# Optimization experiments

Hardware: AMD Instinct MI355X
Metric: run time of the kernel (lower is better)

Reference implementation:

```python
import jax, jax.numpy as jnp
import numpy as np

CH = 256
RED = 4
CQK = CH // RED

def _conv(x, w, b):
    # x: [B,C,H,W], w: [O,I,3,3], b: [O]; SAME padding (pad=1)
    y = jax.lax.conv_general_dilated(
        x, w, window_strides=(1, 1), padding=((1, 1), (1, 1)),
        dimension_numbers=('NCHW', 'OIHW', 'NCHW'))
    return y + b[None, :, None, None]

def setup_inputs() -> dict:
    key = jax.random.key(0)
    ks = jax.random.split(key, 7)
    x = jax.random.normal(ks[0], (4, CH, 64, 64), dtype=jnp.float32)
    fan_in = CH * 9
    s = 1.0 / np.sqrt(fan_in)
    q_w = jax.random.uniform(ks[1], (CQK, CH, 3, 3), jnp.float32, -s, s)
    q_b = jax.random.uniform(ks[2], (CQK,), jnp.float32, -s, s)
    k_w = jax.random.uniform(ks[3], (CQK, CH, 3, 3), jnp.float32, -s, s)
    k_b = jax.random.uniform(ks[4], (CQK,), jnp.float32, -s, s)
    v_w = jax.random.uniform(ks[5], (CH, CH, 3, 3), jnp.float32, -s, s)
    v_b = jax.random.uniform(ks[6], (CH,), jnp.float32, -s, s)
    return {"x": x, "q_w": q_w, "q_b": q_b, "k_w": k_w, "k_b": k_b,
            "v_w": v_w, "v_b": v_b}

def reference(x, q_w, q_b, k_w, k_b, v_w, v_b):
    b, c, h, w = x.shape
    hw = h * w
    scale = CQK ** (-0.5)
    q = _conv(x, q_w, q_b).reshape(b, CQK, hw)   # [B, Cqk, HW]
    k = _conv(x, k_w, k_b).reshape(b, CQK, hw)   # [B, Cqk, HW]
    v = _conv(x, v_w, v_b).reshape(b, c, hw)     # [B, C,   HW]
    # attn[b,i,j] = sum_d q[b,d,i] * k[b,d,j]
    attn = jnp.einsum('bdi,bdj->bij', q, k) * scale
    attn = jax.nn.softmax(attn, axis=-1)         # [B, HW, HW]
    # out[b,c,i] = sum_j v[b,c,j] * attn[b,i,j]  (torch: bmm(v, attn^T))
    out = jnp.einsum('bcj,bij->bci', v, attn).reshape(b, c, h, w)
    return out
```

## Files before the change

### kernel.cpp

```cpp
#include <hip/hip_runtime.h>
#include <stdint.h>

typedef unsigned short u16;
typedef short short8 __attribute__((ext_vector_type(8)));
typedef short short4v __attribute__((ext_vector_type(4)));
typedef float float4v __attribute__((ext_vector_type(4)));
typedef float float16v __attribute__((ext_vector_type(16)));
typedef uint32_t uint2v __attribute__((ext_vector_type(2)));

#define HW 4096
#define QSCL 0.18033688011112042f

#define GLOAD_LDS(g, l) __builtin_amdgcn_global_load_lds( \
    (const __attribute__((address_space(1))) void*)(g),   \
    (__attribute__((address_space(3))) void*)(l), 16, 0, 0)

static __device__ __forceinline__ u16 f2bf(float f) {
  union { float f; uint32_t u; } v; v.f = f;
  uint32_t r = v.u + 0x7fffu + ((v.u >> 16) & 1u);
  return (u16)(r >> 16);
}

static __device__ __forceinline__ uint32_t pkbf(float a, float b) {
  uint32_t r;
  asm("v_cvt_pk_bf16_f32 %0, %1, %2" : "=v"(r) : "v"(a), "v"(b));
  return r;
}
static __device__ __forceinline__ void plswap(uint32_t &a, uint32_t &b) {
  asm("v_permlane32_swap_b32 %0, %1" : "+v"(a), "+v"(b));
}

union PU { uint32_t u[4]; short8 v; };

__global__ __launch_bounds__(256) void k_xt(const float* __restrict__ x, u16* __restrict__ Xtp) {
  __shared__ float t[32][33];
  const int b = blockIdx.z, c0 = blockIdx.y * 32, p0 = blockIdx.x * 32;
  const int tid = threadIdx.x;
  const int l8 = tid >> 5, lp = tid & 31;
#pragma unroll
  for (int i = 0; i < 4; i++) {
    int c = l8 + i * 8;
    t[c][lp] = x[(size_t)(b * 256 + c0 + c) * HW + p0 + lp];
  }
  __syncthreads();
#pragma unroll
  for (int i = 0; i < 4; i++) {
    int p = l8 + i * 8;
    int pp = p0 + p;
    int y = pp >> 6, xx = pp & 63;
    Xtp[((size_t)(b * 66 + y + 1) * 66 + (xx + 1)) * 256 + c0 + lp] = f2bf(t[lp][p]);
  }
}

__global__ __launch_bounds__(256) void k_wprep(const float* __restrict__ qw, const float* __restrict__ qb,
    const float* __restrict__ kw, const float* __restrict__ kb,
    const float* __restrict__ vw, const float* __restrict__ vb,
    u16* __restrict__ Wt, float* __restrict__ bcat) {
  int tid = blockIdx.x * 256 + threadIdx.x;
  if (tid < 9 * 384 * 256) {
    int ci = tid & 255;
    int n = (tid >> 8) % 384;
    int off = tid / (384 * 256);
    float val;
    if (n < 64)       val = qw[(size_t)n * 2304 + ci * 9 + off];
    else if (n < 128) val = kw[(size_t)(n - 64) * 2304 + ci * 9 + off];
    else              val = vw[(size_t)(n - 128) * 2304 + ci * 9 + off];
    Wt[tid] = f2bf(val);
  }
  if (tid < 384) bcat[tid] = (tid < 64) ? qb[tid] : (tid < 128) ? kb[tid - 64] : vb[tid - 128];
}

__global__ __launch_bounds__(256) void k_conv(const u16* __restrict__ Xtp,
    const u16* __restrict__ Wt, const float* __restrict__ bcat,
    u16* __restrict__ Qt, u16* __restrict__ Kt, u16* __restrict__ Vcf) {
  __shared__ __align__(16) u16 Als[2][128 * 64];
  __shared__ __align__(16) u16 Bls[2][64 * 64];
  const int tid = threadIdx.x;
  const int b = blockIdx.z, ct = blockIdx.y;
  const int p0 = blockIdx.x * 128, n0 = ct * 64;
  const int w = tid >> 6, lane = tid & 63, l16 = lane & 15, quad = lane >> 4;

  const int lr = lane >> 3, lcx = (lane & 7) ^ lr;
  const u16* ag[4];
#pragma unroll
  for (int g = 0; g < 4; g++) {
    const int pos = p0 + w * 32 + g * 8 + lr;
    const int py = pos >> 6, px = pos & 63;
    ag[g] = Xtp + ((size_t)(b * 66 + py) * 66 + px) * 256 + lcx * 8;
  }
  const u16* bg[2];
#pragma unroll
  for (int g = 0; g < 2; g++)
    bg[g] = Wt + (size_t)(n0 + w * 16 + g * 8 + lr) * 256 + lcx * 8;

  const int rx = l16 & 7;

  float4v acc[2][4];
  const float4v zz = {0.f, 0.f, 0.f, 0.f};
#pragma unroll
  for (int i = 0; i < 2; i++)
#pragma unroll
    for (int j = 0; j < 4; j++) acc[i][j] = zz;

#pragma unroll
  for (int g = 0; g < 4; g++) GLOAD_LDS(ag[g], &Als[0][(w * 32 + g * 8) * 64]);
#pragma unroll
  for (int g = 0; g < 2; g++) GLOAD_LDS(bg[g], &Bls[0][(w * 16 + g * 8) * 64]);
  __syncthreads();

  for (int ks = 0; ks < 36; ks++) {
    const int buf = ks & 1;
    if (ks + 1 < 36) {
      const int ksn = ks + 1, tap = ksn >> 2, cg = (ksn & 3) * 64;
      const int dy = (tap * 11) >> 5, dx = tap - dy * 3;
      const int aoff = (dy * 66 + dx) * 256 + cg;
      const size_t boff = (size_t)tap * 98304 + cg;
#pragma unroll
      for (int g = 0; g < 4; g++) GLOAD_LDS(ag[g] + aoff, &Als[buf ^ 1][(w * 32 + g * 8) * 64]);
#pragma unroll
      for (int g = 0; g < 2; g++) GLOAD_LDS(bg[g] + boff, &Bls[buf ^ 1][(w * 16 + g * 8) * 64]);
    }

    short8 af[2][2], bfv[4][2];
#pragma unroll
    for (int mt = 0; mt < 2; mt++)
#pragma unroll
      for (int kk = 0; kk < 2; kk++)
        af[mt][kk] = *(const short8*)&Als[buf][(w * 32 + mt * 16 + l16) * 64 + (((kk * 4 + quad) ^ rx) * 8)];
#pragma unroll
    for (int nt = 0; nt < 4; nt++)
#pragma unroll
      for (int kk = 0; kk < 2; kk++)
        bfv[nt][kk] = *(const short8*)&Bls[buf][(nt * 16 + l16) * 64 + (((kk * 4 + quad) ^ rx) * 8)];

    if (ct < 2) {
#pragma unroll
      for (int mt = 0; mt < 2; mt++)
#pragma unroll
        for (int nt = 0; nt < 4; nt++)
#pragma unroll
          for (int kk = 0; kk < 2; kk++)
            acc[mt][nt] = __builtin_amdgcn_mfma_f32_16x16x32_bf16(bfv[nt][kk], af[mt][kk], acc[mt][nt], 0, 0, 0);
    } else {
#pragma unroll
      for (int mt = 0; mt < 2; mt++)
#pragma unroll
        for (int nt = 0; nt < 4; nt++)
#pragma unroll
          for (int kk = 0; kk < 2; kk++)
            acc[mt][nt] = __builtin_amdgcn_mfma_f32_16x16x32_bf16(af[mt][kk], bfv[nt][kk], acc[mt][nt], 0, 0, 0);
    }
    __syncthreads();
  }

  if (ct < 2) {
    u16* base = (ct == 0) ? Qt : Kt;
    const float qs = (ct == 0) ? QSCL : 1.0f;
#pragma unroll
    for (int mt = 0; mt < 2; mt++) {
      const int p = p0 + w * 32 + mt * 16 + l16;
#pragma unroll
      for (int nt = 0; nt < 4; nt++) {
        const int nb = nt * 16 + quad * 4;
        short4v o;
#pragma unroll
        for (int r = 0; r < 4; r++) o[r] = (short)f2bf((acc[mt][nt][r] + bcat[ct * 64 + nb + r]) * qs);
        *(short4v*)(base + (size_t)(b * HW + p) * 64 + nb) = o;
      }
    }
  } else {
#pragma unroll
    for (int mt = 0; mt < 2; mt++) {
      const int pb = p0 + w * 32 + mt * 16 + quad * 4;
#pragma unroll
      for (int nt = 0; nt < 4; nt++) {
        const int cl = nt * 16 + l16;
        const int gc = (ct - 2) * 64 + cl;
        const float bias = bcat[ct * 64 + cl];
        short4v o;
#pragma unroll
        for (int r = 0; r < 4; r++) o[r] = (short)f2bf(acc[mt][nt][r] + bias);
        *(short4v*)(Vcf + (size_t)(b * 256 + gc) * HW + pb) = o;
      }
    }
  }
}

__global__ __launch_bounds__(256, 1) void k_attn(const u16* __restrict__ Qt,
    const u16* __restrict__ Kt, const u16* __restrict__ Vcf, float* __restrict__ out) {
  __shared__ __align__(16) u16 lds[61440];

  const int tid = threadIdx.x;
  const int bid = blockIdx.x;
  const int b = bid & 3;
  const int w = tid >> 6, lane = tid & 63;
  const int l32 = lane & 31, half = lane >> 5;
  const int qa = w & 1, jh = w >> 1;
  const int q0 = (bid >> 2) * 64 + qa * 32;

  u16* Sb = lds + jh * 30720;

  const char* Kgb = (const char*)(Kt + (size_t)b * HW * 64);
  const char* Vgb = (const char*)(Vcf + (size_t)b * 256 * HW);

  const int lr = lane >> 3, lcx = (lane & 7) ^ lr;
  const int vr = lane >> 2, vcx = (lane & 3) ^ ((lane >> 3) & 3);
  const char* ksrc = Kgb + ((size_t)(jh * 2048 + qa * 16 + lr)) * 128 + lcx * 16;
  const char* vsrc = Vgb + ((size_t)(qa * 128 + vr)) * 8192 + (size_t)(jh * 2048) * 2 + vcx * 16;

  short8 qf[4];
  {
    const u16* qp = Qt + ((size_t)(b * HW + q0 + l32)) * 64 + half * 8;
#pragma unroll
    for (int ks = 0; ks < 4; ks++) qf[ks] = *(const short8*)(qp + ks * 16);
  }

  const int sw2 = (l32 >> 1) & 3;
  const int kswz = l32 & 7;

  float16v of[8];
#pragma unroll
  for (int ct = 0; ct < 8; ct++)
#pragma unroll
    for (int r = 0; r < 16; r++) of[ct][r] = 0.f;
  float lp = 0.f;

#define STAGE(T, KS, VS) {                                                        \
    const size_t kb_ = (size_t)(T) * 4096;                                        \
    const size_t vb_ = (size_t)(T) * 64;                                          \
    _Pragma("unroll") for (int g = 0; g < 2; g++)                                 \
      GLOAD_LDS(ksrc + kb_ + g * 1024, &Sb[(KS) + qa * 1024 + g * 512]);          \
    _Pragma("unroll") for (int g = 0; g < 8; g++)                                 \
      GLOAD_LDS(vsrc + vb_ + (size_t)g * 131072, &Sb[(VS) + qa * 4096 + g * 512]);\
  }

#define COMPUTE() {                                                               \
    float16v s;                                                                   \
    _Pragma("unroll") for (int r = 0; r < 16; r++) s[r] = 0.f;                    \
    _Pragma("unroll") for (int ks = 0; ks < 4; ks++) {                            \
      short8 kf = *(const short8*)&Sb[kc + l32 * 64 + (((ks * 2 + half) ^ kswz) * 8)]; \
      s = __builtin_amdgcn_mfma_f32_32x32x16_bf16(kf, qf[ks], s, 0, 0, 0);        \
    }                                                                             \
    float p[16];                                                                  \
    _Pragma("unroll") for (int r = 0; r < 16; r++) p[r] = exp2f(s[r]);            \
    _Pragma("unroll") for (int r = 0; r < 16; r++) lp += p[r];                    \
    uint32_t c0 = pkbf(p[0], p[1]),  c1 = pkbf(p[2], p[3]);                       \
    uint32_t c2 = pkbf(p[4], p[5]),  c3 = pkbf(p[6], p[7]);                       \
    plswap(c0, c2); plswap(c1, c3);                                               \
    uint32_t d0 = pkbf(p[8], p[9]),  d1 = pkbf(p[10], p[11]);                     \
    uint32_t d2 = pkbf(p[12], p[13]), d3 = pkbf(p[14], p[15]);                    \
    plswap(d0, d2); plswap(d1, d3);                                               \
    PU pb0, pb1;                                                                  \
    pb0.u[0] = c0; pb0.u[1] = c1; pb0.u[2] = c2; pb0.u[3] = c3;                   \
    pb1.u[0] = d0; pb1.u[1] = d1; pb1.u[2] = d2; pb1.u[3] = d3;                   \
    _Pragma("unroll") for (int ct = 0; ct < 8; ct++) {                            \
      short8 vf0 = *(const short8*)&Sb[vc + ct * 1024 + l32 * 32 + ((half ^ sw2) * 8)]; \
      of[ct] = __builtin_amdgcn_mfma_f32_32x32x16_bf16(vf0, pb0.v, of[ct], 0, 0, 0);   \
      short8 vf1 = *(const short8*)&Sb[vc + ct * 1024 + l32 * 32 + (((2 + half) ^ sw2) * 8)]; \
      of[ct] = __builtin_amdgcn_mfma_f32_32x32x16_bf16(vf1, pb1.v, of[ct], 0, 0, 0);   \
    }                                                                             \
  }

  int kc = 0, kn = 2048, kt2 = 4096;
  int vc = 6144, vn = 6144 + 8192, vt2 = 6144 + 16384;

  STAGE(0, kc, vc);
  STAGE(1, kn, vn);

  for (int t = 0; t < 63; t++) {
    asm volatile("s_waitcnt vmcnt(10)" ::: "memory");
    __builtin_amdgcn_s_barrier();
    if (t < 62) STAGE(t + 2, kt2, vt2);
    COMPUTE();
    int tk = kc; kc = kn; kn = kt2; kt2 = tk;
    int tv = vc; vc = vn; vn = vt2; vt2 = tv;
  }
  asm volatile("s_waitcnt vmcnt(0)" ::: "memory");
  __builtin_amdgcn_s_barrier();
  COMPUTE();

#undef STAGE
#undef COMPUTE

  lp += __shfl_xor(lp, 32);
  __syncthreads();
  float* Lf = (float*)(lds + 30720);
  if (lane < 32) Lf[w * 32 + l32] = lp;
  float* Osh = (float*)(lds + qa * 30720 + 6144);
  if (jh) {
#pragma unroll
    for (int ct = 0; ct < 8; ct++)
#pragma unroll
      for (int r = 0; r < 16; r++)
        Osh[(ct * 32 + (r & 3) + 8 * (r >> 2) + 4 * half) * 32 + l32] = of[ct][r];
  }
  __syncthreads();
  if (!jh) {
    const float inv = 1.0f / (Lf[qa * 32 + l32] + Lf[(2 + qa) * 32 + l32]);
    float* ob = out + (size_t)b * 256 * HW + q0 + l32;
#pragma unroll
    for (int ct = 0; ct < 8; ct++)
#pragma unroll
      for (int r = 0; r < 16; r++) {
        const int c = ct * 32 + (r & 3) + 8 * (r >> 2) + 4 * half;
        ob[(size_t)c * HW] = (of[ct][r] + Osh[c * 32 + l32]) * inv;
      }
  }
}

extern "C" void kernel_launch(void* const* d_in, const int* in_sizes, int n_in,
                              void* d_out, int out_size, void* d_ws, size_t ws_size,
                              hipStream_t stream) {
  const float* x  = (const float*)d_in[0];
  const float* qw = (const float*)d_in[1];
  const float* qb = (const float*)d_in[2];
  const float* kw = (const float*)d_in[3];
  const float* kb = (const float*)d_in[4];
  const float* vw = (const float*)d_in[5];
  const float* vb = (const float*)d_in[6];
  float* out = (float*)d_out;
  char* ws = (char*)d_ws;
  u16*   Xtp = (u16*)(ws);
  u16*   Wt  = (u16*)(ws + 8921088);
  float* bc  = (float*)(ws + 10690560);
  u16*   Qt  = (u16*)(ws + 10692096);
  u16*   Kt  = (u16*)(ws + 12789248);
  u16*   Vcf = (u16*)(ws + 14886400);

  hipMemsetAsync(Xtp, 0, 8921088, stream);
  k_xt  <<<dim3(128, 8, 4), 256, 0, stream>>>(x, Xtp);
  k_wprep<<<3456, 256, 0, stream>>>(qw, qb, kw, kb, vw, vb, Wt, bc);
  k_conv<<<dim3(32, 6, 4), 256, 0, stream>>>(Xtp, Wt, bc, Qt, Kt, Vcf);
  k_attn<<<256, 256, 0, stream>>>(Qt, Kt, Vcf, out);
}
```

Measured before the change: 194.5 us.

## Load K fragments directly to registers and double-buffer larger V tiles

Restructures the attention main loop. K fragments are now loaded straight from global memory into registers two tiles ahead, instead of being staged through LDS. Each iteration handles 64 keys, computing two score tiles, and only V goes through double-buffered LDS with an XOR swizzle. This halves the number of barriers per key range and removes K LDS traffic, at the cost of more registers for the K fragments and bigger V staging per step.

```diff
diff --git a/kernel.cpp b/kernel.cpp
--- a/kernel.cpp
+++ b/kernel.cpp
@@ -188,35 +188,33 @@
 
 __global__ __launch_bounds__(256, 1) void k_attn(const u16* __restrict__ Qt,
     const u16* __restrict__ Kt, const u16* __restrict__ Vcf, float* __restrict__ out) {
-  __shared__ __align__(16) u16 lds[61440];
+  __shared__ __align__(16) u16 lds[65536];
 
   const int tid = threadIdx.x;
   const int bid = blockIdx.x;
   const int b = bid & 3;
+  const int q0 = (bid >> 2) * 64;
   const int w = tid >> 6, lane = tid & 63;
   const int l32 = lane & 31, half = lane >> 5;
   const int qa = w & 1, jh = w >> 1;
-  const int q0 = (bid >> 2) * 64 + qa * 32;
-
-  u16* Sb = lds + jh * 30720;
-
-  const char* Kgb = (const char*)(Kt + (size_t)b * HW * 64);
-  const char* Vgb = (const char*)(Vcf + (size_t)b * 256 * HW);
+
+  u16* Sv = lds + jh * 32768;
 
   const int lr = lane >> 3, lcx = (lane & 7) ^ lr;
-  const int vr = lane >> 2, vcx = (lane & 3) ^ ((lane >> 3) & 3);
-  const char* ksrc = Kgb + ((size_t)(jh * 2048 + qa * 16 + lr)) * 128 + lcx * 16;
-  const char* vsrc = Vgb + ((size_t)(qa * 128 + vr)) * 8192 + (size_t)(jh * 2048) * 2 + vcx * 16;
+  const char* vs0 = (const char*)Vcf + ((size_t)(b * 256 + qa * 128 + lr)) * 8192
+                    + jh * 4096 + (size_t)lcx * 16;
+
+  const u16* kq = Kt + ((size_t)(b * HW + jh * 2048 + l32)) * 64 + half * 8;
 
   short8 qf[4];
   {
-    const u16* qp = Qt + ((size_t)(b * HW + q0 + l32)) * 64 + half * 8;
+    const u16* qp = Qt + ((size_t)(b * HW + q0 + qa * 32 + l32)) * 64 + half * 8;
 #pragma unroll
     for (int ks = 0; ks < 4; ks++) qf[ks] = *(const short8*)(qp + ks * 16);
   }
 
-  const int sw2 = (l32 >> 1) & 3;
-  const int kswz = l32 & 7;
+  const int rx = l32 & 7;
+  const int vrow = l32 * 64;
 
   float16v of[8];
 #pragma unroll
@@ -225,68 +223,83 @@
     for (int r = 0; r < 16; r++) of[ct][r] = 0.f;
   float lp = 0.f;
 
-#define STAGE(T, KS, VS) {                                                        \
-    const size_t kb_ = (size_t)(T) * 4096;                                        \
-    const size_t vb_ = (size_t)(T) * 64;                                          \
-    _Pragma("unroll") for (int g = 0; g < 2; g++)                                 \
-      GLOAD_LDS(ksrc + kb_ + g * 1024, &Sb[(KS) + qa * 1024 + g * 512]);          \
-    _Pragma("unroll") for (int g = 0; g < 8; g++)                                 \
-      GLOAD_LDS(vsrc + vb_ + (size_t)g * 131072, &Sb[(VS) + qa * 4096 + g * 512]);\
-  }
-
-#define COMPUTE() {                                                               \
-    float16v s;                                                                   \
-    _Pragma("unroll") for (int r = 0; r < 16; r++) s[r] = 0.f;                    \
+  short8 kfA[2][4], kfB[2][4];
+
+#define STAGEV(T, BUF) {                                                          \
+    const char* vt = vs0 + (size_t)(T) * 128;                                     \
+    u16* db = Sv + (BUF) * 16384 + qa * 8192;                                     \
+    _Pragma("unroll") for (int g = 0; g < 16; g++)                                \
+      GLOAD_LDS(vt + (size_t)g * 65536, db + g * 512);                            \
+  }
+
+#define LOADK(T, KF) {                                                            \
+    const u16* kp = kq + (size_t)((T) & 31) * 4096;                               \
+    _Pragma("unroll") for (int js = 0; js < 2; js++)                              \
+      _Pragma("unroll") for (int ks = 0; ks < 4; ks++)                            \
+        KF[js][ks] = *(const short8*)(kp + js * 2048 + ks * 16);                  \
+  }
+
+#define SOFTPV(SS, VB, C0, C1) {                                                  \
+    float p0 = exp2f(SS[0]),  p1 = exp2f(SS[1]),  p2 = exp2f(SS[2]),  p3 = exp2f(SS[3]);   \
+    float p4 = exp2f(SS[4]),  p5 = exp2f(SS[5]),  p6 = exp2f(SS[6]),  p7 = exp2f(SS[7]);   \
+    float p8 = exp2f(SS[8]),  p9 = exp2f(SS[9]),  pa = exp2f(SS[10]), pb_ = exp2f(SS[11]); \
+    float pc = exp2f(SS[12]), pd = exp2f(SS[13]), pe = exp2f(SS[14]), pf = exp2f(SS[15]);  \
+    lp += ((p0 + p1) + (p2 + p3)) + ((p4 + p5) + (p6 + p7))                       \
+        + ((p8 + p9) + (pa + pb_)) + ((pc + pd) + (pe + pf));                     \
+    uint32_t c0 = pkbf(p0, p1), c1 = pkbf(p2, p3), c2 = pkbf(p4, p5), c3 = pkbf(p6, p7);   \
+    plswap(c0, c2); plswap(c1, c3);                                               \
+    uint32_t d0 = pkbf(p8, p9), d1 = pkbf(pa, pb_), d2 = pkbf(pc, pd), d3 = pkbf(pe, pf);  \
+    plswap(d0, d2); plswap(d1, d3);                                               \
+    PU pA, pB;                                                                    \
+    pA.u[0] = c0; pA.u[1] = c1; pA.u[2] = c2; pA.u[3] = c3;                       \
+    pB.u[0] = d0; pB.u[1] = d1; pB.u[2] = d2; pB.u[3] = d3;                       \
+    const int ca = (((C0) + half) ^ rx) * 8, cb = (((C1) + half) ^ rx) * 8;       \
+    _Pragma("unroll") for (int ct = 0; ct < 8; ct++) {                            \
+      short8 vfa = *(const short8*)&VB[vrow + ct * 2048 + ca];                    \
+      of[ct] = __builtin_amdgcn_mfma_f32_32x32x16_bf16(vfa, pA.v, of[ct], 0, 0, 0); \
+      short8 vfb = *(const short8*)&VB[vrow + ct * 2048 + cb];                    \
+      of[ct] = __builtin_amdgcn_mfma_f32_32x32x16_bf16(vfb, pB.v, of[ct], 0, 0, 0); \
+    }                                                                             \
+  }
+
+#define HALF_ITER(T, PAR, KF) {                                                   \
+    asm volatile("s_waitcnt vmcnt(8)" ::: "memory");                              \
+    __builtin_amdgcn_s_barrier();                                                 \
+    __builtin_amdgcn_sched_barrier(0);                                            \
+    STAGEV(((T) + 1) & 31, (PAR) ^ 1);                                            \
+    __builtin_amdgcn_sched_barrier(0);                                            \
+    float16v s0, s1;                                                              \
+    _Pragma("unroll") for (int r = 0; r < 16; r++) { s0[r] = 0.f; s1[r] = 0.f; }  \
     _Pragma("unroll") for (int ks = 0; ks < 4; ks++) {                            \
-      short8 kf = *(const short8*)&Sb[kc + l32 * 64 + (((ks * 2 + half) ^ kswz) * 8)]; \
-      s = __builtin_amdgcn_mfma_f32_32x32x16_bf16(kf, qf[ks], s, 0, 0, 0);        \
+      s0 = __builtin_amdgcn_mfma_f32_32x32x16_bf16(KF[0][ks], qf[ks], s0, 0, 0, 0); \
+      s1 = __builtin_amdgcn_mfma_f32_32x32x16_bf16(KF[1][ks], qf[ks], s1, 0, 0, 0); \
     }                                                                             \
-    float p[16];                                                                  \
-    _Pragma("unroll") for (int r = 0; r < 16; r++) p[r] = exp2f(s[r]);            \
-    _Pragma("unroll") for (int r = 0; r < 16; r++) lp += p[r];                    \
-    uint32_t c0 = pkbf(p[0], p[1]),  c1 = pkbf(p[2], p[3]);                       \
-    uint32_t c2 = pkbf(p[4], p[5]),  c3 = pkbf(p[6], p[7]);                       \
-    plswap(c0, c2); plswap(c1, c3);                                               \
-    uint32_t d0 = pkbf(p[8], p[9]),  d1 = pkbf(p[10], p[11]);                     \
-    uint32_t d2 = pkbf(p[12], p[13]), d3 = pkbf(p[14], p[15]);                    \
-    plswap(d0, d2); plswap(d1, d3);                                               \
-    PU pb0, pb1;                                                                  \
-    pb0.u[0] = c0; pb0.u[1] = c1; pb0.u[2] = c2; pb0.u[3] = c3;                   \
-    pb1.u[0] = d0; pb1.u[1] = d1; pb1.u[2] = d2; pb1.u[3] = d3;                   \
-    _Pragma("unroll") for (int ct = 0; ct < 8; ct++) {                            \
-      short8 vf0 = *(const short8*)&Sb[vc + ct * 1024 + l32 * 32 + ((half ^ sw2) * 8)]; \
-      of[ct] = __builtin_amdgcn_mfma_f32_32x32x16_bf16(vf0, pb0.v, of[ct], 0, 0, 0);   \
-      short8 vf1 = *(const short8*)&Sb[vc + ct * 1024 + l32 * 32 + (((2 + half) ^ sw2) * 8)]; \
-      of[ct] = __builtin_amdgcn_mfma_f32_32x32x16_bf16(vf1, pb1.v, of[ct], 0, 0, 0);   \
-    }                                                                             \
-  }
-
-  int kc = 0, kn = 2048, kt2 = 4096;
-  int vc = 6144, vn = 6144 + 8192, vt2 = 6144 + 16384;
-
-  STAGE(0, kc, vc);
-  STAGE(1, kn, vn);
-
-  for (int t = 0; t < 63; t++) {
-    asm volatile("s_waitcnt vmcnt(10)" ::: "memory");
-    __builtin_amdgcn_s_barrier();
-    if (t < 62) STAGE(t + 2, kt2, vt2);
-    COMPUTE();
-    int tk = kc; kc = kn; kn = kt2; kt2 = tk;
-    int tv = vc; vc = vn; vn = vt2; vt2 = tv;
-  }
-  asm volatile("s_waitcnt vmcnt(0)" ::: "memory");
-  __builtin_amdgcn_s_barrier();
-  COMPUTE();
-
-#undef STAGE
-#undef COMPUTE
+    LOADK((T) + 2, KF);                                                           \
+    __builtin_amdgcn_sched_barrier(0);                                            \
+    const u16* VB = Sv + (PAR) * 16384;                                           \
+    SOFTPV(s0, VB, 0, 2);                                                         \
+    SOFTPV(s1, VB, 4, 6);                                                         \
+  }
+
+  STAGEV(0, 0);
+  __builtin_amdgcn_sched_barrier(0);
+  LOADK(0, kfA);
+  LOADK(1, kfB);
+
+  for (int t = 0; t < 32; t += 2) {
+    HALF_ITER(t, 0, kfA);
+    HALF_ITER(t + 1, 1, kfB);
+  }
+#undef HALF_ITER
+#undef SOFTPV
+#undef LOADK
+#undef STAGEV
 
   lp += __shfl_xor(lp, 32);
   __syncthreads();
-  float* Lf = (float*)(lds + 30720);
+  float* Lf = (float*)lds + 16384;
   if (lane < 32) Lf[w * 32 + l32] = lp;
-  float* Osh = (float*)(lds + qa * 30720 + 6144);
+  float* Osh = (float*)lds + qa * 8192;
   if (jh) {
 #pragma unroll
     for (int ct = 0; ct < 8; ct++)
@@ -297,7 +310,7 @@
   __syncthreads();
   if (!jh) {
     const float inv = 1.0f / (Lf[qa * 32 + l32] + Lf[(2 + qa) * 32 + l32]);
-    float* ob = out + (size_t)b * 256 * HW + q0 + l32;
+    float* ob = out + (size_t)(b * 256) * HW + q0 + qa * 32 + l32;
 #pragma unroll
     for (int ct = 0; ct < 8; ct++)
 #pragma unroll
```

New measurement: 225.2 us. +15.7%, slower.

## Split attention key range across blocks and reduce partial outputs in a separate kernel

Applied to the files above, without the earlier changes.

The attention kernel now launches 512 blocks of 512 threads. Each block handles one batch, one half of the key range and 64 queries, and each wave owns 64 output channels instead of all 256. The much smaller per-wave accumulator should allow higher occupancy with double-buffered LDS. Partial unnormalized outputs and row sums are written to workspace and combined in a new reduce kernel. The cost is extra global traffic (about 32 MB of fp32 partials written and read back), one more launch, and the QK^T scores being recomputed for each channel group of waves.

```diff
diff --git a/kernel.cpp b/kernel.cpp
--- a/kernel.cpp
+++ b/kernel.cpp
@@ -186,126 +186,120 @@
   }
 }
 
-__global__ __launch_bounds__(256, 1) void k_attn(const u16* __restrict__ Qt,
-    const u16* __restrict__ Kt, const u16* __restrict__ Vcf, float* __restrict__ out) {
-  __shared__ __align__(16) u16 lds[61440];
-
-  const int tid = threadIdx.x;
-  const int bid = blockIdx.x;
+__global__ __launch_bounds__(512, 4) void k_attn(const u16* __restrict__ Qt,
+    const u16* __restrict__ Kt, const u16* __restrict__ Vcf,
+    float* __restrict__ Opart, float* __restrict__ Lpart) {
+  __shared__ __align__(16) u16 Vls[2][8192];
+  __shared__ __align__(16) u16 Kls[2][2048];
+
+  const int tid = threadIdx.x, bid = blockIdx.x;
   const int b = bid & 3;
+  const int jh = (bid >> 2) & 1, it = bid >> 3;
   const int w = tid >> 6, lane = tid & 63;
   const int l32 = lane & 31, half = lane >> 5;
-  const int qa = w & 1, jh = w >> 1;
-  const int q0 = (bid >> 2) * 64 + qa * 32;
-
-  u16* Sb = lds + jh * 30720;
-
-  const char* Kgb = (const char*)(Kt + (size_t)b * HW * 64);
-  const char* Vgb = (const char*)(Vcf + (size_t)b * 256 * HW);
-
+  const int qa = w & 1, cs = w >> 1;
+
+  const int vr = lane >> 2, vcx = (lane & 3) ^ (vr & 3);
   const int lr = lane >> 3, lcx = (lane & 7) ^ lr;
-  const int vr = lane >> 2, vcx = (lane & 3) ^ ((lane >> 3) & 3);
-  const char* ksrc = Kgb + ((size_t)(jh * 2048 + qa * 16 + lr)) * 128 + lcx * 16;
-  const char* vsrc = Vgb + ((size_t)(qa * 128 + vr)) * 8192 + (size_t)(jh * 2048) * 2 + vcx * 16;
+  const char* vsrc = (const char*)Vcf + ((size_t)(b * 256 + w * 32 + vr)) * 8192
+                     + jh * 4096 + vcx * 16;
+  const char* ksrc = (const char*)Kt + ((size_t)(b * HW + jh * 2048 + (w & 3) * 8 + lr)) * 128
+                     + lcx * 16;
 
   short8 qf[4];
   {
-    const u16* qp = Qt + ((size_t)(b * HW + q0 + l32)) * 64 + half * 8;
+    const u16* qp = Qt + ((size_t)(b * HW + it * 64 + qa * 32 + l32)) * 64 + half * 8;
 #pragma unroll
     for (int ks = 0; ks < 4; ks++) qf[ks] = *(const short8*)(qp + ks * 16);
   }
 
-  const int sw2 = (l32 >> 1) & 3;
-  const int kswz = l32 & 7;
-
-  float16v of[8];
-#pragma unroll
-  for (int ct = 0; ct < 8; ct++)
-#pragma unroll
-    for (int r = 0; r < 16; r++) of[ct][r] = 0.f;
+  const int rxk = l32 & 7, rxv = l32 & 3;
+  const int krow = l32 * 64;
+  const int vrow0 = (cs * 64 + l32) * 32;
+
+  float16v of0, of1;
+#pragma unroll
+  for (int r = 0; r < 16; r++) { of0[r] = 0.f; of1[r] = 0.f; }
   float lp = 0.f;
 
-#define STAGE(T, KS, VS) {                                                        \
-    const size_t kb_ = (size_t)(T) * 4096;                                        \
-    const size_t vb_ = (size_t)(T) * 64;                                          \
-    _Pragma("unroll") for (int g = 0; g < 2; g++)                                 \
-      GLOAD_LDS(ksrc + kb_ + g * 1024, &Sb[(KS) + qa * 1024 + g * 512]);          \
-    _Pragma("unroll") for (int g = 0; g < 8; g++)                                 \
-      GLOAD_LDS(vsrc + vb_ + (size_t)g * 131072, &Sb[(VS) + qa * 4096 + g * 512]);\
-  }
-
-#define COMPUTE() {                                                               \
+#define STAGE(T, BUF) {                                                           \
+    GLOAD_LDS(vsrc + (size_t)(T) * 64, &Vls[BUF][(w * 32) * 32]);                 \
+    GLOAD_LDS(vsrc + (size_t)(T) * 64 + 16 * 8192, &Vls[BUF][(w * 32 + 16) * 32]);\
+    GLOAD_LDS(ksrc + (size_t)(T) * 4096, &Kls[BUF][(w & 3) * 512]);               \
+  }
+
+#define COMPUTE(BUF) {                                                            \
     float16v s;                                                                   \
     _Pragma("unroll") for (int r = 0; r < 16; r++) s[r] = 0.f;                    \
     _Pragma("unroll") for (int ks = 0; ks < 4; ks++) {                            \
-      short8 kf = *(const short8*)&Sb[kc + l32 * 64 + (((ks * 2 + half) ^ kswz) * 8)]; \
+      short8 kf = *(const short8*)&Kls[BUF][krow + (((ks * 2 + half) ^ rxk) * 8)];\
       s = __builtin_amdgcn_mfma_f32_32x32x16_bf16(kf, qf[ks], s, 0, 0, 0);        \
     }                                                                             \
-    float p[16];                                                                  \
-    _Pragma("unroll") for (int r = 0; r < 16; r++) p[r] = exp2f(s[r]);            \
-    _Pragma("unroll") for (int r = 0; r < 16; r++) lp += p[r];                    \
-    uint32_t c0 = pkbf(p[0], p[1]),  c1 = pkbf(p[2], p[3]);                       \
-    uint32_t c2 = pkbf(p[4], p[5]),  c3 = pkbf(p[6], p[7]);                       \
+    float p0 = exp2f(s[0]),  p1 = exp2f(s[1]),  p2 = exp2f(s[2]),  p3 = exp2f(s[3]);   \
+    float p4 = exp2f(s[4]),  p5 = exp2f(s[5]),  p6 = exp2f(s[6]),  p7 = exp2f(s[7]);   \
+    float p8 = exp2f(s[8]),  p9 = exp2f(s[9]),  pa = exp2f(s[10]), pb_ = exp2f(s[11]); \
+    float pc = exp2f(s[12]), pd = exp2f(s[13]), pe = exp2f(s[14]), pf = exp2f(s[15]);  \
+    lp += ((p0 + p1) + (p2 + p3)) + ((p4 + p5) + (p6 + p7))                       \
+        + ((p8 + p9) + (pa + pb_)) + ((pc + pd) + (pe + pf));                     \
+    uint32_t c0 = pkbf(p0, p1), c1 = pkbf(p2, p3), c2 = pkbf(p4, p5), c3 = pkbf(p6, p7);   \
     plswap(c0, c2); plswap(c1, c3);                                               \
-    uint32_t d0 = pkbf(p[8], p[9]),  d1 = pkbf(p[10], p[11]);                     \
-    uint32_t d2 = pkbf(p[12], p[13]), d3 = pkbf(p[14], p[15]);                    \
+    uint32_t d0 = pkbf(p8, p9), d1 = pkbf(pa, pb_), d2 = pkbf(pc, pd), d3 = pkbf(pe, pf);  \
     plswap(d0, d2); plswap(d1, d3);                                               \
-    PU pb0, pb1;                                                                  \
-    pb0.u[0] = c0; pb0.u[1] = c1; pb0.u[2] = c2; pb0.u[3] = c3;                   \
-    pb1.u[0] = d0; pb1.u[1] = d1; pb1.u[2] = d2; pb1.u[3] = d3;                   \
-    _Pragma("unroll") for (int ct = 0; ct < 8; ct++) {                            \
-      short8 vf0 = *(const short8*)&Sb[vc + ct * 1024 + l32 * 32 + ((half ^ sw2) * 8)]; \
-      of[ct] = __builtin_amdgcn_mfma_f32_32x32x16_bf16(vf0, pb0.v, of[ct], 0, 0, 0);   \
-      short8 vf1 = *(const short8*)&Sb[vc + ct * 1024 + l32 * 32 + (((2 + half) ^ sw2) * 8)]; \
-      of[ct] = __builtin_amdgcn_mfma_f32_32x32x16_bf16(vf1, pb1.v, of[ct], 0, 0, 0);   \
-    }                                                                             \
-  }
-
-  int kc = 0, kn = 2048, kt2 = 4096;
-  int vc = 6144, vn = 6144 + 8192, vt2 = 6144 + 16384;
-
-  STAGE(0, kc, vc);
-  STAGE(1, kn, vn);
-
-  for (int t = 0; t < 63; t++) {
-    asm volatile("s_waitcnt vmcnt(10)" ::: "memory");
-    __builtin_amdgcn_s_barrier();
-    if (t < 62) STAGE(t + 2, kt2, vt2);
-    COMPUTE();
-    int tk = kc; kc = kn; kn = kt2; kt2 = tk;
-    int tv = vc; vc = vn; vn = vt2; vt2 = tv;
-  }
-  asm volatile("s_waitcnt vmcnt(0)" ::: "memory");
-  __builtin_amdgcn_s_barrier();
-  COMPUTE();
-
+    PU pA, pB;                                                                    \
+    pA.u[0] = c0; pA.u[1] = c1; pA.u[2] = c2; pA.u[3] = c3;                       \
+    pB.u[0] = d0; pB.u[1] = d1; pB.u[2] = d2; pB.u[3] = d3;                       \
+    const int ca = ((half ^ rxv) * 8), cb = (((2 + half) ^ rxv) * 8);             \
+    short8 va0 = *(const short8*)&Vls[BUF][vrow0 + ca];                           \
+    of0 = __builtin_amdgcn_mfma_f32_32x32x16_bf16(va0, pA.v, of0, 0, 0, 0);       \
+    short8 vb0 = *(const short8*)&Vls[BUF][vrow0 + cb];                           \
+    of0 = __builtin_amdgcn_mfma_f32_32x32x16_bf16(vb0, pB.v, of0, 0, 0, 0);       \
+    short8 va1 = *(const short8*)&Vls[BUF][vrow0 + 1024 + ca];                    \
+    of1 = __builtin_amdgcn_mfma_f32_32x32x16_bf16(va1, pA.v, of1, 0, 0, 0);       \
+    short8 vb1 = *(const short8*)&Vls[BUF][vrow0 + 1024 + cb];                    \
+    of1 = __builtin_amdgcn_mfma_f32_32x32x16_bf16(vb1, pB.v, of1, 0, 0, 0);       \
+  }
+
+  STAGE(0, 0);
+  __syncthreads();
+
+  for (int t = 0; t < 64; t++) {
+    const int buf = t & 1;
+    if (t < 63) STAGE(t + 1, buf ^ 1);
+    COMPUTE(buf);
+    __syncthreads();
+  }
+#undef COMPUTE
 #undef STAGE
-#undef COMPUTE
 
   lp += __shfl_xor(lp, 32);
-  __syncthreads();
-  float* Lf = (float*)(lds + 30720);
-  if (lane < 32) Lf[w * 32 + l32] = lp;
-  float* Osh = (float*)(lds + qa * 30720 + 6144);
-  if (jh) {
-#pragma unroll
-    for (int ct = 0; ct < 8; ct++)
-#pragma unroll
-      for (int r = 0; r < 16; r++)
-        Osh[(ct * 32 + (r & 3) + 8 * (r >> 2) + 4 * half) * 32 + l32] = of[ct][r];
-  }
-  __syncthreads();
-  if (!jh) {
-    const float inv = 1.0f / (Lf[qa * 32 + l32] + Lf[(2 + qa) * 32 + l32]);
-    float* ob = out + (size_t)b * 256 * HW + q0 + l32;
-#pragma unroll
-    for (int ct = 0; ct < 8; ct++)
-#pragma unroll
-      for (int r = 0; r < 16; r++) {
-        const int c = ct * 32 + (r & 3) + 8 * (r >> 2) + 4 * half;
-        ob[(size_t)c * HW] = (of[ct][r] + Osh[c * 32 + l32]) * inv;
-      }
-  }
+  float* Ob = Opart + ((size_t)(jh * 4 + b) * 256) * 4096 + it * 64 + qa * 32 + l32;
+#pragma unroll
+  for (int ct = 0; ct < 2; ct++) {
+    const float16v o = ct ? of1 : of0;
+#pragma unroll
+    for (int r = 0; r < 16; r++) {
+      const int c = cs * 64 + ct * 32 + (r & 3) + 8 * (r >> 2) + 4 * half;
+      Ob[(size_t)c * 4096] = o[r];
+    }
+  }
+  if (cs == 0 && lane < 32)
+    Lpart[(size_t)(jh * 4 + b) * 4096 + it * 64 + qa * 32 + l32] = lp;
+}
+
+__global__ __launch_bounds__(256) void k_reduce(const float* __restrict__ Op,
+    const float* __restrict__ Lp, float* __restrict__ out) {
+  const int idx = blockIdx.x * 256 + threadIdx.x;
+  const size_t f0 = (size_t)idx * 4;
+  const int i = (int)(f0 & 4095);
+  const int b = (int)(f0 >> 20);
+  float4v o0 = *(const float4v*)(Op + f0);
+  float4v o1 = *(const float4v*)(Op + f0 + 4194304);
+  float4v l0 = *(const float4v*)(Lp + (size_t)b * 4096 + i);
+  float4v l1 = *(const float4v*)(Lp + (size_t)(4 + b) * 4096 + i);
+  float4v r;
+#pragma unroll
+  for (int k = 0; k < 4; k++) r[k] = (o0[k] + o1[k]) * (1.0f / (l0[k] + l1[k]));
+  *(float4v*)(out + f0) = r;
 }
 
 extern "C" void kernel_launch(void* const* d_in, const int* in_sizes, int n_in,
@@ -326,10 +320,13 @@
   u16*   Qt  = (u16*)(ws + 10692096);
   u16*   Kt  = (u16*)(ws + 12789248);
   u16*   Vcf = (u16*)(ws + 14886400);
+  float* Op  = (float*)(ws + 23275008);
+  float* Lp  = (float*)(ws + 56829440);
 
   hipMemsetAsync(Xtp, 0, 8921088, stream);
   k_xt  <<<dim3(128, 8, 4), 256, 0, stream>>>(x, Xtp);
   k_wprep<<<3456, 256, 0, stream>>>(qw, qb, kw, kb, vw, vb, Wt, bc);
   k_conv<<<dim3(32, 6, 4), 256, 0, stream>>>(Xtp, Wt, bc, Qt, Kt, Vcf);
-  k_attn<<<256, 256, 0, stream>>>(Qt, Kt, Vcf, out);
-}
+  k_attn<<<512, 512, 0, stream>>>(Qt, Kt, Vcf, Op, Lp);
+  k_reduce<<<4096, 256, 0, stream>>>(Op, Lp, out);
+}
```

After: 242.2 us. 24.5% more time.
